# Kernel optimization log

Hardware: AMD Instinct MI355X
Metric: run time of the kernel (lower is better)

## Reference

```python
import jax, jax.numpy as jnp
import numpy as np

B, T, S = 1, 8, 1024
HID, H = 1152, 16
D = HID // H  # 72
EPS = 1e-6


def rmsnorm(t, gamma):
    # t: [b,t,s,h,d], gamma: [h,d] per-head learnable scale (QKNorm)
    var = jnp.mean(jnp.square(t), axis=-1, keepdims=True)
    return t * jax.lax.rsqrt(var + EPS) * gamma


def setup_inputs() -> dict:
    key = jax.random.key(0)
    ks = jax.random.split(key, 8)
    sc = lambda fan_in: 1.0 / np.sqrt(fan_in)
    x = jax.random.normal(ks[0], (B, T, S, HID), dtype=jnp.float32)
    Wq = jax.random.normal(ks[1], (HID, HID), dtype=jnp.float32) * sc(HID)
    bq = jnp.zeros((HID,), dtype=jnp.float32)
    Wkv = jax.random.normal(ks[2], (HID, 2 * HID), dtype=jnp.float32) * sc(HID)
    bkv = jnp.zeros((2 * HID,), dtype=jnp.float32)
    q_gamma = jnp.ones((H, D), dtype=jnp.float32)
    k_gamma = jnp.ones((H, D), dtype=jnp.float32)
    Wo = jax.random.normal(ks[3], (HID, HID), dtype=jnp.float32) * sc(HID)
    return {"x": x, "Wq": Wq, "bq": bq, "Wkv": Wkv, "bkv": bkv,
            "q_gamma": q_gamma, "k_gamma": k_gamma, "Wo": Wo}


def reference(x, Wq, bq, Wkv, bkv, q_gamma, k_gamma, Wo):
    b, t, s, _ = x.shape
    q = (x @ Wq + bq).reshape(b, t, s, H, D)
    kv = x @ Wkv + bkv
    k, v = jnp.split(kv, 2, axis=-1)
    k = k.reshape(b, t, s, H, D)
    v = v.reshape(b, t, s, H, D)
    q = rmsnorm(q, q_gamma)
    k = rmsnorm(k, k_gamma)
    # NOTE: original applies no 1/sqrt(d) scaling (QKNorm replaces it)
    attn_weight = jnp.einsum('btqhd,btkhd->bthqk', q, k)
    attn = jax.nn.softmax(attn_weight, axis=-1)
    out = jnp.einsum('bthqk,btkhd->btqhd', attn, v).reshape(b, t, s, HID)
    return out @ Wo
```

## Files before the change

### kernel.cpp

```cpp
#include <hip/hip_runtime.h>


typedef __attribute__((ext_vector_type(4))) short s16x4;
typedef __attribute__((ext_vector_type(8))) short s16x8;
typedef __attribute__((ext_vector_type(4))) float f32x4;

__device__ __forceinline__ unsigned short f2b(float x) {
  unsigned u = __float_as_uint(x);
  u += 0x7FFFu + ((u >> 16) & 1u);
  return (unsigned short)(u >> 16);
}
__device__ __forceinline__ float b2f(unsigned short u) {
  return __uint_as_float(((unsigned)u) << 16);
}

__global__ __launch_bounds__(256) void cvt_bf16_kernel(const float* __restrict__ in,
                                                       unsigned short* __restrict__ out,
                                                       int n8) {
  int i = blockIdx.x * 256 + threadIdx.x;
  if (i >= n8) return;
  const float4* p = (const float4*)(in + (size_t)i * 8);
  float4 a = p[0], b = p[1];
  s16x8 r;
  r[0] = (short)f2b(a.x); r[1] = (short)f2b(a.y); r[2] = (short)f2b(a.z); r[3] = (short)f2b(a.w);
  r[4] = (short)f2b(b.x); r[5] = (short)f2b(b.y); r[6] = (short)f2b(b.z); r[7] = (short)f2b(b.w);
  *(s16x8*)(out + (size_t)i * 8) = r;
}

__global__ __launch_bounds__(256) void transpose_cvt_kernel(const float* __restrict__ W,
                                                            unsigned short* __restrict__ WT,
                                                            int K, int N) {
  __shared__ float tile[32][33];
  int n0 = blockIdx.x * 32, k0 = blockIdx.y * 32;
  int tx = threadIdx.x, ty = threadIdx.y;
#pragma unroll
  for (int i = 0; i < 4; i++)
    tile[ty + i * 8][tx] = W[(size_t)(k0 + ty + i * 8) * N + n0 + tx];
  __syncthreads();
#pragma unroll
  for (int i = 0; i < 4; i++)
    WT[(size_t)(n0 + ty + i * 8) * K + k0 + tx] = f2b(tile[tx][ty + i * 8]);
}

template <int MODE>
__global__ __launch_bounds__(256) void gemm_bt_kernel(const unsigned short* __restrict__ A,
                                                      const unsigned short* __restrict__ BT,
                                                      const float* __restrict__ biasq,
                                                      const float* __restrict__ biaskv,
                                                      int N, int gx,
                                                      float* __restrict__ outF,
                                                      unsigned short* __restrict__ qn,
                                                      unsigned short* __restrict__ kn,
                                                      unsigned short* __restrict__ vt) {
  constexpr int K = 1152;
  constexpr int NT = K / 32;
  __shared__ unsigned short As[2][128][40];
  __shared__ unsigned short Bs[2][128][40];
  int tid = threadIdx.x;
  int lane = tid & 63, wave = tid >> 6;
  int wr = (wave >> 1) * 64, wc = (wave & 1) * 64;
  int l15 = lane & 15, lq = lane >> 4, kf = lq * 4;
  int nwg = gridDim.x;
  int bid = blockIdx.x;
  int wgid = (bid & 7) * (nwg >> 3) + (bid >> 3);
  int bx = wgid % gx, by = wgid / gx;
  int brow = by * 128, bcol = bx * 128;
  int row0 = tid >> 2, col0 = (tid & 3) * 8;
  int row1 = row0 + 64;
  const unsigned short* Ag0 = A + (size_t)(brow + row0) * K + col0;
  const unsigned short* Ag1 = A + (size_t)(brow + row1) * K + col0;
  const unsigned short* Bg0 = BT + (size_t)(bcol + row0) * K + col0;
  const unsigned short* Bg1 = BT + (size_t)(bcol + row1) * K + col0;
  s16x8 ra0, ra1, rb0, rb1;
  ra0 = *(const s16x8*)Ag0;
  ra1 = *(const s16x8*)Ag1;
  rb0 = *(const s16x8*)Bg0;
  rb1 = *(const s16x8*)Bg1;
  *(s16x8*)&As[0][row0][col0] = ra0;
  *(s16x8*)&As[0][row1][col0] = ra1;
  *(s16x8*)&Bs[0][row0][col0] = rb0;
  *(s16x8*)&Bs[0][row1][col0] = rb1;
  f32x4 acc[4][4] = {};
  for (int kt = 0; kt < NT; kt++) {
    __syncthreads();
    int cur = kt & 1;
    if (kt < NT - 1) {
      int off = (kt + 1) * 32;
      ra0 = *(const s16x8*)(Ag0 + off);
      ra1 = *(const s16x8*)(Ag1 + off);
      rb0 = *(const s16x8*)(Bg0 + off);
      rb1 = *(const s16x8*)(Bg1 + off);
    }
    s16x8 af[4], bf[4];
#pragma unroll
    for (int m = 0; m < 4; m++) {
      s16x4 lo = *(const s16x4*)&As[cur][wr + m * 16 + l15][kf];
      s16x4 hi = *(const s16x4*)&As[cur][wr + m * 16 + l15][kf + 16];
      af[m] = __builtin_shufflevector(lo, hi, 0, 1, 2, 3, 4, 5, 6, 7);
      s16x4 blo = *(const s16x4*)&Bs[cur][wc + m * 16 + l15][kf];
      s16x4 bhi = *(const s16x4*)&Bs[cur][wc + m * 16 + l15][kf + 16];
      bf[m] = __builtin_shufflevector(blo, bhi, 0, 1, 2, 3, 4, 5, 6, 7);
    }
    __builtin_amdgcn_s_setprio(1);
#pragma unroll
    for (int m = 0; m < 4; m++)
#pragma unroll
      for (int n = 0; n < 4; n++)
        acc[m][n] = __builtin_amdgcn_mfma_f32_16x16x32_bf16(af[m], bf[n], acc[m][n], 0, 0, 0);
    __builtin_amdgcn_s_setprio(0);
    if (kt < NT - 1) {
      int nxt = cur ^ 1;
      *(s16x8*)&As[nxt][row0][col0] = ra0;
      *(s16x8*)&As[nxt][row1][col0] = ra1;
      *(s16x8*)&Bs[nxt][row0][col0] = rb0;
      *(s16x8*)&Bs[nxt][row1][col0] = rb1;
    }
  }
#pragma unroll
  for (int m = 0; m < 4; m++) {
#pragma unroll
    for (int n = 0; n < 4; n++) {
#pragma unroll
      for (int r = 0; r < 4; r++) {
        int grow = brow + wr + m * 16 + lq * 4 + r;
        int gcol = bcol + wc + n * 16 + l15;
        float v = acc[m][n][r];
        if (MODE == 0) {
          outF[(size_t)grow * N + gcol] = v;
        } else {
          v += (gcol < 1152) ? biasq[gcol] : biaskv[gcol - 1152];
          int t = grow >> 10, s = grow & 1023;
          if (gcol < 2304) {
            int c = (gcol < 1152) ? gcol : gcol - 1152;
            int h = c / 72, d = c - h * 72;
            unsigned short* dst = (gcol < 1152) ? qn : kn;
            dst[((size_t)((t * 16 + h) * 1024 + s)) * 96 + d] = f2b(v);
          } else {
            int c = gcol - 2304;
            int h = c / 72, d = c - h * 72;
            vt[((size_t)((t * 16 + h) * 80 + d)) * 1024 + s] = f2b(v);
          }
        }
      }
    }
  }
}

__global__ __launch_bounds__(256) void rmsnorm2_kernel(unsigned short* __restrict__ qn,
                                                       unsigned short* __restrict__ kn,
                                                       const float* __restrict__ qg,
                                                       const float* __restrict__ kg) {
  int r = blockIdx.x * 4 + (threadIdx.x >> 6);
  int isK = r >= 131072;
  int g = isK ? r - 131072 : r;
  unsigned short* buf = isK ? kn : qn;
  const float* gamma = isK ? kg : qg;
  int h = (g >> 10) & 15;
  size_t base = (size_t)g * 96;
  int l = threadIdx.x & 63;
  float e0 = b2f(buf[base + l]);
  float e1 = 0.f;
  if (l < 8) e1 = b2f(buf[base + 64 + l]);
  float ss = e0 * e0 + e1 * e1;
#pragma unroll
  for (int m = 1; m < 64; m <<= 1) ss += __shfl_xor(ss, m);
  float sc = rsqrtf(ss * (1.0f / 72.0f) + 1e-6f);
  buf[base + l] = f2b(e0 * sc * gamma[h * 72 + l]);
  if (l < 32) {
    float v = 0.f;
    if (l < 8) v = e1 * sc * gamma[h * 72 + 64 + l];
    buf[base + 64 + l] = f2b(v);
  }
}

__global__ __launch_bounds__(256) void attn_kernel(const unsigned short* __restrict__ Qn,
                                                   const unsigned short* __restrict__ Kn,
                                                   const unsigned short* __restrict__ VtG,
                                                   unsigned short* __restrict__ att) {
  __shared__ unsigned short Kl[2][64][100];
  __shared__ unsigned short Vt[2][80][76];
  int tid = threadIdx.x;
  int lane = tid & 63, wave = tid >> 6;
  int l15 = lane & 15, lq = lane >> 4, kf = lq * 4;
  int bid = blockIdx.x;
  int orig = (bid & 7) * 256 + (bid >> 3);
  int qb = orig & 15, th = orig >> 4;
  int t = th >> 4, h = th & 15;
  const unsigned short* Q = Qn + (size_t)th * 1024 * 96;
  const unsigned short* Kp = Kn + (size_t)th * 1024 * 96;
  const unsigned short* Vg = VtG + (size_t)th * 80 * 1024;
  int qrow0 = qb * 64 + wave * 16;
  int krow[3], kco[3], vd[3], vco[3];
#pragma unroll
  for (int i = 0; i < 3; i++) {
    int c = tid + i * 256;
    krow[i] = c / 12;
    kco[i] = c - 12 * krow[i];
    int cc = tid + i * 256;
    vd[i] = cc >> 3;
    vco[i] = cc & 7;
  }
  bool v2 = tid < 128;
  s16x8 sk[3], sv[3];
  s16x8 qf[3];
#pragma unroll
  for (int c = 0; c < 3; c++) {
    const unsigned short* p = Q + (size_t)(qrow0 + l15) * 96 + c * 32 + kf;
    s16x4 lo = *(const s16x4*)p;
    s16x4 hi = *(const s16x4*)(p + 16);
    qf[c] = __builtin_shufflevector(lo, hi, 0, 1, 2, 3, 4, 5, 6, 7);
  }
  f32x4 o[5] = {};
  float m_r = -3.0e38f, l_r = 0.f;

#pragma unroll
  for (int i = 0; i < 3; i++)
    sk[i] = *(const s16x8*)(Kp + (size_t)krow[i] * 96 + kco[i] * 8);
#pragma unroll
  for (int i = 0; i < 2; i++)
    sv[i] = *(const s16x8*)(Vg + (size_t)vd[i] * 1024 + vco[i] * 8);
  if (v2) sv[2] = *(const s16x8*)(Vg + (size_t)vd[2] * 1024 + vco[2] * 8);
#pragma unroll
  for (int i = 0; i < 3; i++) *(s16x8*)&Kl[0][krow[i]][kco[i] * 8] = sk[i];
#pragma unroll
  for (int i = 0; i < 2; i++) *(s16x8*)&Vt[0][vd[i]][vco[i] * 8] = sv[i];
  if (v2) *(s16x8*)&Vt[0][vd[2]][vco[2] * 8] = sv[2];

  for (int tt = 0; tt < 16; tt++) {
    __syncthreads();
    int cur = tt & 1;
    if (tt < 15) {
      int kv1 = (tt + 1) * 64;
#pragma unroll
      for (int i = 0; i < 3; i++)
        sk[i] = *(const s16x8*)(Kp + (size_t)(kv1 + krow[i]) * 96 + kco[i] * 8);
#pragma unroll
      for (int i = 0; i < 2; i++)
        sv[i] = *(const s16x8*)(Vg + (size_t)vd[i] * 1024 + kv1 + vco[i] * 8);
      if (v2) sv[2] = *(const s16x8*)(Vg + (size_t)vd[2] * 1024 + kv1 + vco[2] * 8);
    }
    f32x4 st[4];
    __builtin_amdgcn_s_setprio(1);
#pragma unroll
    for (int n = 0; n < 4; n++) {
      f32x4 a = {};
#pragma unroll
      for (int c = 0; c < 3; c++) {
        s16x4 lo = *(const s16x4*)&Kl[cur][n * 16 + l15][c * 32 + kf];
        s16x4 hi = *(const s16x4*)&Kl[cur][n * 16 + l15][c * 32 + kf + 16];
        s16x8 kfr = __builtin_shufflevector(lo, hi, 0, 1, 2, 3, 4, 5, 6, 7);
        a = __builtin_amdgcn_mfma_f32_16x16x32_bf16(kfr, qf[c], a, 0, 0, 0);
      }
      st[n] = a;
    }
    __builtin_amdgcn_s_setprio(0);
    float tmax = st[0][0];
#pragma unroll
    for (int n = 0; n < 4; n++)
#pragma unroll
      for (int r = 0; r < 4; r++) tmax = fmaxf(tmax, st[n][r]);
    tmax = fmaxf(tmax, __shfl_xor(tmax, 16));
    tmax = fmaxf(tmax, __shfl_xor(tmax, 32));
    float mn = fmaxf(m_r, tmax);
    float scale = __expf(m_r - mn);
    m_r = mn;
    float sum = 0.f;
#pragma unroll
    for (int n = 0; n < 4; n++)
#pragma unroll
      for (int r = 0; r < 4; r++) {
        float p = __expf(st[n][r] - mn);
        st[n][r] = p;
        sum += p;
      }
    sum += __shfl_xor(sum, 16);
    sum += __shfl_xor(sum, 32);
    l_r = l_r * scale + sum;
#pragma unroll
    for (int r = 0; r < 4; r++) {
      float scq = __shfl(scale, 4 * lq + r);
#pragma unroll
      for (int v = 0; v < 5; v++) o[v][r] *= scq;
    }
    __builtin_amdgcn_s_setprio(1);
#pragma unroll
    for (int b = 0; b < 2; b++) {
      s16x8 pf;
#pragma unroll
      for (int j = 0; j < 8; j++) pf[j] = (short)f2b(st[2 * b + (j >> 2)][j & 3]);
#pragma unroll
      for (int v = 0; v < 5; v++) {
        s16x4 vlo = *(const s16x4*)&Vt[cur][v * 16 + l15][b * 32 + kf];
        s16x4 vhi = *(const s16x4*)&Vt[cur][v * 16 + l15][b * 32 + kf + 16];
        s16x8 vf = __builtin_shufflevector(vlo, vhi, 0, 1, 2, 3, 4, 5, 6, 7);
        o[v] = __builtin_amdgcn_mfma_f32_16x16x32_bf16(pf, vf, o[v], 0, 0, 0);
      }
    }
    __builtin_amdgcn_s_setprio(0);
    if (tt < 15) {
      int nxt = cur ^ 1;
#pragma unroll
      for (int i = 0; i < 3; i++) *(s16x8*)&Kl[nxt][krow[i]][kco[i] * 8] = sk[i];
#pragma unroll
      for (int i = 0; i < 2; i++) *(s16x8*)&Vt[nxt][vd[i]][vco[i] * 8] = sv[i];
      if (v2) *(s16x8*)&Vt[nxt][vd[2]][vco[2] * 8] = sv[2];
    }
  }
#pragma unroll
  for (int r = 0; r < 4; r++) {
    float inv = 1.0f / __shfl(l_r, 4 * lq + r);
    int qrow = qrow0 + 4 * lq + r;
    size_t rowbase = (size_t)(t * 1024 + qrow) * 1152 + h * 72;
#pragma unroll
    for (int v = 0; v < 5; v++) {
      int d = v * 16 + l15;
      if (d < 72) att[rowbase + d] = f2b(o[v][r] * inv);
    }
  }
}

extern "C" void kernel_launch(void* const* d_in, const int* in_sizes, int n_in,
                              void* d_out, int out_size, void* d_ws, size_t ws_size,
                              hipStream_t stream) {
  const float* x   = (const float*)d_in[0];
  const float* Wq  = (const float*)d_in[1];
  const float* bq  = (const float*)d_in[2];
  const float* Wkv = (const float*)d_in[3];
  const float* bkv = (const float*)d_in[4];
  const float* qg  = (const float*)d_in[5];
  const float* kg  = (const float*)d_in[6];
  const float* Wo  = (const float*)d_in[7];
  float* out = (float*)d_out;

  char* w = (char*)d_ws;
  unsigned short* xb   = (unsigned short*)w; w += (size_t)8192 * 1152 * 2;
  unsigned short* WqT  = (unsigned short*)w; w += (size_t)1152 * 1152 * 2;
  unsigned short* WkvT = (unsigned short*)w; w += (size_t)2304 * 1152 * 2;
  unsigned short* WoT  = (unsigned short*)w; w += (size_t)1152 * 1152 * 2;
  unsigned short* qn   = (unsigned short*)w; w += (size_t)128 * 1024 * 96 * 2;
  unsigned short* kn   = (unsigned short*)w; w += (size_t)128 * 1024 * 96 * 2;
  unsigned short* vt   = (unsigned short*)w; w += (size_t)128 * 80 * 1024 * 2;
  unsigned short* att  = (unsigned short*)w; w += (size_t)8192 * 1152 * 2;

  cvt_bf16_kernel<<<4608, 256, 0, stream>>>(x, xb, 9437184 / 8);
  transpose_cvt_kernel<<<dim3(36, 36), dim3(32, 8), 0, stream>>>(Wq, WqT, 1152, 1152);
  transpose_cvt_kernel<<<dim3(72, 36), dim3(32, 8), 0, stream>>>(Wkv, WkvT, 1152, 2304);
  transpose_cvt_kernel<<<dim3(36, 36), dim3(32, 8), 0, stream>>>(Wo, WoT, 1152, 1152);

  gemm_bt_kernel<3><<<1728, 256, 0, stream>>>(xb, WqT, bq, bkv, 3456, 27, nullptr, qn, kn, vt);
  rmsnorm2_kernel<<<65536, 256, 0, stream>>>(qn, kn, qg, kg);

  attn_kernel<<<2048, 256, 0, stream>>>(qn, kn, vt, att);

  gemm_bt_kernel<0><<<576, 256, 0, stream>>>(att, WoT, nullptr, nullptr, 1152, 9, out, nullptr, nullptr, nullptr);
}
```

Measured before the change: 336.7 us.

## Load GEMM tiles directly to LDS with global_load_lds and XOR swizzle

Replaces the register-staged global-to-LDS copy in the bf16 GEMM with direct global_load_lds (16-byte) transfers into an unpadded, XOR-swizzled LDS layout. Fragment reads use matching swizzled offsets. The aim is to save VGPRs and the ds_write instructions, and to avoid bank conflicts without padding. In exchange, each iteration now waits on vmcnt(0) before the barrier, which may reduce overlap between the prefetch and compute.

```diff
diff --git a/kernel.cpp b/kernel.cpp
--- a/kernel.cpp
+++ b/kernel.cpp
@@ -12,6 +12,11 @@
 }
 __device__ __forceinline__ float b2f(unsigned short u) {
   return __uint_as_float(((unsigned)u) << 16);
+}
+__device__ __forceinline__ void gld16(const void* g, void* l) {
+  __builtin_amdgcn_global_load_lds(
+      (const __attribute__((address_space(1))) void*)g,
+      (__attribute__((address_space(3))) void*)l, 16, 0, 0);
 }
 
 __global__ __launch_bounds__(256) void cvt_bf16_kernel(const float* __restrict__ in,
@@ -54,51 +59,55 @@
                                                       unsigned short* __restrict__ vt) {
   constexpr int K = 1152;
   constexpr int NT = K / 32;
-  __shared__ unsigned short As[2][128][40];
-  __shared__ unsigned short Bs[2][128][40];
+  __shared__ __align__(16) unsigned short As[2][4096];
+  __shared__ __align__(16) unsigned short Bs[2][4096];
   int tid = threadIdx.x;
   int lane = tid & 63, wave = tid >> 6;
   int wr = (wave >> 1) * 64, wc = (wave & 1) * 64;
-  int l15 = lane & 15, lq = lane >> 4, kf = lq * 4;
+  int l15 = lane & 15, lq = lane >> 4;
   int nwg = gridDim.x;
   int bid = blockIdx.x;
   int wgid = (bid & 7) * (nwg >> 3) + (bid >> 3);
   int bx = wgid % gx, by = wgid / gx;
   int brow = by * 128, bcol = bx * 128;
-  int row0 = tid >> 2, col0 = (tid & 3) * 8;
-  int row1 = row0 + 64;
-  const unsigned short* Ag0 = A + (size_t)(brow + row0) * K + col0;
-  const unsigned short* Ag1 = A + (size_t)(brow + row1) * K + col0;
-  const unsigned short* Bg0 = BT + (size_t)(bcol + row0) * K + col0;
-  const unsigned short* Bg1 = BT + (size_t)(bcol + row1) * K + col0;
-  s16x8 ra0, ra1, rb0, rb1;
-  ra0 = *(const s16x8*)Ag0;
-  ra1 = *(const s16x8*)Ag1;
-  rb0 = *(const s16x8*)Bg0;
-  rb1 = *(const s16x8*)Bg1;
-  *(s16x8*)&As[0][row0][col0] = ra0;
-  *(s16x8*)&As[0][row1][col0] = ra1;
-  *(s16x8*)&Bs[0][row0][col0] = rb0;
-  *(s16x8*)&Bs[0][row1][col0] = rb1;
+  int r0 = tid >> 2;
+  int c0 = (((tid & 3) ^ (r0 & 3)) << 3);
+  const unsigned short* Ag0 = A + (size_t)(brow + r0) * K + c0;
+  const unsigned short* Ag1 = A + (size_t)(brow + r0 + 64) * K + c0;
+  const unsigned short* Bg0 = BT + (size_t)(bcol + r0) * K + c0;
+  const unsigned short* Bg1 = BT + (size_t)(bcol + r0 + 64) * K + c0;
+  int ldsL = wave * 512;
+  int ldsH = 2048 + wave * 512;
+  int xa = l15 & 3;
+  int loff = (((lq >> 1) ^ xa) << 3) + ((lq & 1) << 2);
+  int hoff = ((((lq >> 1) | 2) ^ xa) << 3) + ((lq & 1) << 2);
+  gld16(Ag0, &As[0][ldsL]);
+  gld16(Ag1, &As[0][ldsH]);
+  gld16(Bg0, &Bs[0][ldsL]);
+  gld16(Bg1, &Bs[0][ldsH]);
   f32x4 acc[4][4] = {};
   for (int kt = 0; kt < NT; kt++) {
+    asm volatile("s_waitcnt vmcnt(0)" ::: "memory");
     __syncthreads();
     int cur = kt & 1;
     if (kt < NT - 1) {
       int off = (kt + 1) * 32;
-      ra0 = *(const s16x8*)(Ag0 + off);
-      ra1 = *(const s16x8*)(Ag1 + off);
-      rb0 = *(const s16x8*)(Bg0 + off);
-      rb1 = *(const s16x8*)(Bg1 + off);
+      int nxt = cur ^ 1;
+      gld16(Ag0 + off, &As[nxt][ldsL]);
+      gld16(Ag1 + off, &As[nxt][ldsH]);
+      gld16(Bg0 + off, &Bs[nxt][ldsL]);
+      gld16(Bg1 + off, &Bs[nxt][ldsH]);
     }
     s16x8 af[4], bf[4];
 #pragma unroll
     for (int m = 0; m < 4; m++) {
-      s16x4 lo = *(const s16x4*)&As[cur][wr + m * 16 + l15][kf];
-      s16x4 hi = *(const s16x4*)&As[cur][wr + m * 16 + l15][kf + 16];
+      int ra = (wr + m * 16 + l15) * 32;
+      s16x4 lo = *(const s16x4*)&As[cur][ra + loff];
+      s16x4 hi = *(const s16x4*)&As[cur][ra + hoff];
       af[m] = __builtin_shufflevector(lo, hi, 0, 1, 2, 3, 4, 5, 6, 7);
-      s16x4 blo = *(const s16x4*)&Bs[cur][wc + m * 16 + l15][kf];
-      s16x4 bhi = *(const s16x4*)&Bs[cur][wc + m * 16 + l15][kf + 16];
+      int rb = (wc + m * 16 + l15) * 32;
+      s16x4 blo = *(const s16x4*)&Bs[cur][rb + loff];
+      s16x4 bhi = *(const s16x4*)&Bs[cur][rb + hoff];
       bf[m] = __builtin_shufflevector(blo, bhi, 0, 1, 2, 3, 4, 5, 6, 7);
     }
     __builtin_amdgcn_s_setprio(1);
@@ -108,13 +117,6 @@
       for (int n = 0; n < 4; n++)
         acc[m][n] = __builtin_amdgcn_mfma_f32_16x16x32_bf16(af[m], bf[n], acc[m][n], 0, 0, 0);
     __builtin_amdgcn_s_setprio(0);
-    if (kt < NT - 1) {
-      int nxt = cur ^ 1;
-      *(s16x8*)&As[nxt][row0][col0] = ra0;
-      *(s16x8*)&As[nxt][row1][col0] = ra1;
-      *(s16x8*)&Bs[nxt][row0][col0] = rb0;
-      *(s16x8*)&Bs[nxt][row1][col0] = rb1;
-    }
   }
 #pragma unroll
   for (int m = 0; m < 4; m++) {
@@ -122,7 +124,7 @@
     for (int n = 0; n < 4; n++) {
 #pragma unroll
       for (int r = 0; r < 4; r++) {
-        int grow = brow + wr + m * 16 + lq * 4 + r;
+        int grow = brow + wr + m * 16 + (lq << 2) + r;
         int gcol = bcol + wc + n * 16 + l15;
         float v = acc[m][n][r];
         if (MODE == 0) {
```

Result: slower. 386.0 us (+14.6%).

## Deepen GEMM global prefetch to two stages and remap blocks per XCD

Applied to the files above, without the earlier changes.

The GEMM main loop is unrolled by two and keeps two register sets of prefetched tiles, so global loads are issued two K-steps ahead instead of one and have more latency to hide. Block-to-tile mapping is replaced with a fixed per-XCD grouping (8 row tiles by 3 column tiles per XCD group) aimed at better L2 reuse of A and B tiles. The cost is extra registers, and the hard-coded mapping assumes a specific grid shape (64 row tiles, column tiles divisible by 3), which works only if every launch of both modes fits that shape.

```diff
diff --git a/kernel.cpp b/kernel.cpp
--- a/kernel.cpp
+++ b/kernel.cpp
@@ -60,10 +60,13 @@
   int lane = tid & 63, wave = tid >> 6;
   int wr = (wave >> 1) * 64, wc = (wave & 1) * 64;
   int l15 = lane & 15, lq = lane >> 4, kf = lq * 4;
-  int nwg = gridDim.x;
   int bid = blockIdx.x;
-  int wgid = (bid & 7) * (nwg >> 3) + (bid >> 3);
-  int bx = wgid % gx, by = wgid / gx;
+  int xcd = bid & 7;
+  int w = bid >> 3;
+  int st = w / 24, inner = w - st * 24;
+  int ibx = inner % 3, iby = inner / 3;
+  int bx = st * 3 + ibx;
+  int by = xcd * 8 + iby;
   int brow = by * 128, bcol = bx * 128;
   int row0 = tid >> 2, col0 = (tid & 3) * 8;
   int row1 = row0 + 64;
@@ -71,51 +74,70 @@
   const unsigned short* Ag1 = A + (size_t)(brow + row1) * K + col0;
   const unsigned short* Bg0 = BT + (size_t)(bcol + row0) * K + col0;
   const unsigned short* Bg1 = BT + (size_t)(bcol + row1) * K + col0;
-  s16x8 ra0, ra1, rb0, rb1;
-  ra0 = *(const s16x8*)Ag0;
-  ra1 = *(const s16x8*)Ag1;
-  rb0 = *(const s16x8*)Bg0;
-  rb1 = *(const s16x8*)Bg1;
-  *(s16x8*)&As[0][row0][col0] = ra0;
-  *(s16x8*)&As[0][row1][col0] = ra1;
-  *(s16x8*)&Bs[0][row0][col0] = rb0;
-  *(s16x8*)&Bs[0][row1][col0] = rb1;
+  s16x8 pa0, pa1, pb0, pb1;
+  s16x8 qa0, qa1, qb0, qb1;
+  pa0 = *(const s16x8*)Ag0;
+  pa1 = *(const s16x8*)Ag1;
+  pb0 = *(const s16x8*)Bg0;
+  pb1 = *(const s16x8*)Bg1;
+  *(s16x8*)&As[0][row0][col0] = pa0;
+  *(s16x8*)&As[0][row1][col0] = pa1;
+  *(s16x8*)&Bs[0][row0][col0] = pb0;
+  *(s16x8*)&Bs[0][row1][col0] = pb1;
+  qa0 = *(const s16x8*)(Ag0 + 32);
+  qa1 = *(const s16x8*)(Ag1 + 32);
+  qb0 = *(const s16x8*)(Bg0 + 32);
+  qb1 = *(const s16x8*)(Bg1 + 32);
   f32x4 acc[4][4] = {};
-  for (int kt = 0; kt < NT; kt++) {
+#define GEMM_COMPUTE(CUR)                                                        \
+  {                                                                              \
+    s16x8 af[4], bf[4];                                                          \
+    _Pragma("unroll") for (int m = 0; m < 4; m++) {                              \
+      s16x4 lo = *(const s16x4*)&As[CUR][wr + m * 16 + l15][kf];                 \
+      s16x4 hi = *(const s16x4*)&As[CUR][wr + m * 16 + l15][kf + 16];            \
+      af[m] = __builtin_shufflevector(lo, hi, 0, 1, 2, 3, 4, 5, 6, 7);           \
+      s16x4 blo = *(const s16x4*)&Bs[CUR][wc + m * 16 + l15][kf];                \
+      s16x4 bhi = *(const s16x4*)&Bs[CUR][wc + m * 16 + l15][kf + 16];           \
+      bf[m] = __builtin_shufflevector(blo, bhi, 0, 1, 2, 3, 4, 5, 6, 7);         \
+    }                                                                            \
+    __builtin_amdgcn_s_setprio(1);                                               \
+    _Pragma("unroll") for (int m = 0; m < 4; m++)                                \
+        _Pragma("unroll") for (int n = 0; n < 4; n++)                            \
+            acc[m][n] =                                                          \
+        __builtin_amdgcn_mfma_f32_16x16x32_bf16(af[m], bf[n], acc[m][n], 0, 0, 0); \
+    __builtin_amdgcn_s_setprio(0);                                               \
+  }
+  for (int kt = 0; kt < NT; kt += 2) {
     __syncthreads();
-    int cur = kt & 1;
-    if (kt < NT - 1) {
-      int off = (kt + 1) * 32;
-      ra0 = *(const s16x8*)(Ag0 + off);
-      ra1 = *(const s16x8*)(Ag1 + off);
-      rb0 = *(const s16x8*)(Bg0 + off);
-      rb1 = *(const s16x8*)(Bg1 + off);
-    }
-    s16x8 af[4], bf[4];
-#pragma unroll
-    for (int m = 0; m < 4; m++) {
-      s16x4 lo = *(const s16x4*)&As[cur][wr + m * 16 + l15][kf];
-      s16x4 hi = *(const s16x4*)&As[cur][wr + m * 16 + l15][kf + 16];
-      af[m] = __builtin_shufflevector(lo, hi, 0, 1, 2, 3, 4, 5, 6, 7);
-      s16x4 blo = *(const s16x4*)&Bs[cur][wc + m * 16 + l15][kf];
-      s16x4 bhi = *(const s16x4*)&Bs[cur][wc + m * 16 + l15][kf + 16];
-      bf[m] = __builtin_shufflevector(blo, bhi, 0, 1, 2, 3, 4, 5, 6, 7);
-    }
-    __builtin_amdgcn_s_setprio(1);
-#pragma unroll
-    for (int m = 0; m < 4; m++)
-#pragma unroll
-      for (int n = 0; n < 4; n++)
-        acc[m][n] = __builtin_amdgcn_mfma_f32_16x16x32_bf16(af[m], bf[n], acc[m][n], 0, 0, 0);
-    __builtin_amdgcn_s_setprio(0);
-    if (kt < NT - 1) {
-      int nxt = cur ^ 1;
-      *(s16x8*)&As[nxt][row0][col0] = ra0;
-      *(s16x8*)&As[nxt][row1][col0] = ra1;
-      *(s16x8*)&Bs[nxt][row0][col0] = rb0;
-      *(s16x8*)&Bs[nxt][row1][col0] = rb1;
-    }
-  }
+    if (kt + 2 < NT) {
+      int off = (kt + 2) * 32;
+      pa0 = *(const s16x8*)(Ag0 + off);
+      pa1 = *(const s16x8*)(Ag1 + off);
+      pb0 = *(const s16x8*)(Bg0 + off);
+      pb1 = *(const s16x8*)(Bg1 + off);
+    }
+    GEMM_COMPUTE(0);
+    *(s16x8*)&As[1][row0][col0] = qa0;
+    *(s16x8*)&As[1][row1][col0] = qa1;
+    *(s16x8*)&Bs[1][row0][col0] = qb0;
+    *(s16x8*)&Bs[1][row1][col0] = qb1;
+    __syncthreads();
+    if (kt + 3 < NT) {
+      int off = (kt + 3) * 32;
+      qa0 = *(const s16x8*)(Ag0 + off);
+      qa1 = *(const s16x8*)(Ag1 + off);
+      qb0 = *(const s16x8*)(Bg0 + off);
+      qb1 = *(const s16x8*)(Bg1 + off);
+    }
+    GEMM_COMPUTE(1);
+    if (kt + 2 < NT) {
+      *(s16x8*)&As[0][row0][col0] = pa0;
+      *(s16x8*)&As[0][row1][col0] = pa1;
+      *(s16x8*)&Bs[0][row0][col0] = pb0;
+      *(s16x8*)&Bs[0][row1][col0] = pb1;
+    }
+  }
+#undef GEMM_COMPUTE
 #pragma unroll
   for (int m = 0; m < 4; m++) {
 #pragma unroll
```

After: 334.4 us. Within noise of the previous version (-0.7%).
